# Optimization experiments

Hardware: AMD Instinct MI355X
Metric: run time of the kernel (lower is better)

The kernel has to match this reference:

```python
import jax, jax.numpy as jnp
import numpy as np

N = 500000
C_IN = 32
C_OUT = 64
K = 9  # neighbors per node


def setup_inputs() -> dict:
    key = jax.random.key(0)
    k1, k2, k3, k4 = jax.random.split(key, 4)
    features = jax.random.normal(k1, (N, C_IN), dtype=jnp.float32)
    # neighbor indices in [-1, N); -1 marks missing neighbor (zero-padded)
    neigh_idx = jax.random.randint(k2, (N, K), -1, N, dtype=jnp.int64)
    W = jax.random.normal(k3, (C_OUT, K * C_IN), dtype=jnp.float32) / np.sqrt(K * C_IN)
    b = jax.random.normal(k4, (C_OUT,), dtype=jnp.float32) * 0.01
    return {"features": features, "neigh_idx": neigh_idx, "W": W, "b": b}


def reference(features, neigh_idx, W, b):
    n = neigh_idx.shape[0]
    # append zero sentinel row at index n (matches torch cat with pad_vec)
    feat_padded = jnp.concatenate(
        [features, jnp.zeros((1, features.shape[1]), dtype=features.dtype)], axis=0
    )
    gather_idx = jnp.where(neigh_idx == -1, n, neigh_idx)
    gathered = feat_padded[gather_idx].reshape(n, -1)  # [N, 9*C]
    return gathered @ W.T + b
```

## Files before the change

### kernel.cpp

```cpp
#include <hip/hip_runtime.h>
#include <hip/hip_bf16.h>


typedef __bf16 bf16x8 __attribute__((ext_vector_type(8)));
typedef float  f32x16 __attribute__((ext_vector_type(16)));
typedef float  f32x4  __attribute__((ext_vector_type(4)));
typedef unsigned short ushort8 __attribute__((ext_vector_type(8)));

#define NPB 128

__global__ __launch_bounds__(256) void cvt_bf16_kernel(
    const float* __restrict__ src, __bf16* __restrict__ dst, long long total)
{
    long long stride = (long long)gridDim.x * 256 * 8;
    for (long long i = ((long long)blockIdx.x * 256 + threadIdx.x) * 8;
         i + 7 < total; i += stride) {
        f32x4 f0 = __builtin_nontemporal_load((const f32x4*)(src + i));
        f32x4 f1 = __builtin_nontemporal_load((const f32x4*)(src + i + 4));
        bf16x8 v;
        v[0] = (__bf16)f0[0]; v[1] = (__bf16)f0[1]; v[2] = (__bf16)f0[2]; v[3] = (__bf16)f0[3];
        v[4] = (__bf16)f1[0]; v[5] = (__bf16)f1[1]; v[6] = (__bf16)f1[2]; v[7] = (__bf16)f1[3];
        *(bf16x8*)(dst + i) = v;
    }
}

template<bool FAST>
__global__ __launch_bounds__(512, 8) void quadconv_kernel(
    const float*  __restrict__ feat,
    const __bf16* __restrict__ fb,
    const int*    __restrict__ nidx,
    const float*  __restrict__ Wm,
    const float*  __restrict__ bias,
    float*        __restrict__ out,
    int N)
{
    __shared__ __bf16 Wl[2304 * 8];

    const int tid  = threadIdx.x;
    const int lane = tid & 63;
    const int w    = tid >> 6;

    #pragma unroll
    for (int i = 0; i < 5; ++i) {
        int c = tid + i * 512;
        if (c < 2304) {
            int kk   = c >> 7;
            int r    = c & 127;
            int half = r >> 6;
            int l    = r & 63;
            int row  = half * 32 + (l & 31);
            int col0 = kk * 16 + (l >> 5) * 8;
            const float* wp = Wm + row * 288 + col0;
            f32x4 w0 = *(const f32x4*)(wp);
            f32x4 w1 = *(const f32x4*)(wp + 4);
            bf16x8 v;
            v[0] = (__bf16)w0[0]; v[1] = (__bf16)w0[1]; v[2] = (__bf16)w0[2]; v[3] = (__bf16)w0[3];
            v[4] = (__bf16)w1[0]; v[5] = (__bf16)w1[1]; v[6] = (__bf16)w1[2]; v[7] = (__bf16)w1[3];
            *(bf16x8*)&Wl[c * 8] = v;
        }
    }

    const int half    = w & 1;
    const int nodeOff = (w >> 1) * 32;
    const int klane   = (lane >> 5) * 8;
    const long long nbase = (long long)blockIdx.x * NPB + nodeOff;
    const long long row   = nbase + (lane & 31);
    const bool valid = row < (long long)N;

    const float bv = bias[half * 32 + (lane & 31)];

    int idxs[9];
    #pragma unroll
    for (int j = 0; j < 9; ++j)
        idxs[j] = valid ? nidx[row * 9 + j] : -1;

    __syncthreads();

    f32x16 acc;
    #pragma unroll
    for (int i = 0; i < 16; ++i) acc[i] = 0.0f;

    bf16x8 zvec;
    #pragma unroll
    for (int i = 0; i < 8; ++i) zvec[i] = (__bf16)0.0f;

    #pragma unroll 1
    for (int g = 0; g < 3; ++g) {
        bf16x8 a[6];
        #pragma unroll
        for (int jj = 0; jj < 3; ++jj) {
            int id = idxs[g * 3 + jj];
            #pragma unroll
            for (int h = 0; h < 2; ++h) {
                bf16x8 v = zvec;
                if (id >= 0) {
                    if (FAST) {
                        v = *(const bf16x8*)(fb + (long long)id * 32 + h * 16 + klane);
                    } else {
                        const float* sp = feat + (long long)id * 32 + h * 16 + klane;
                        f32x4 f0 = *(const f32x4*)(sp);
                        f32x4 f1 = *(const f32x4*)(sp + 4);
                        v[0] = (__bf16)f0[0]; v[1] = (__bf16)f0[1]; v[2] = (__bf16)f0[2]; v[3] = (__bf16)f0[3];
                        v[4] = (__bf16)f1[0]; v[5] = (__bf16)f1[1]; v[6] = (__bf16)f1[2]; v[7] = (__bf16)f1[3];
                    }
                }
                a[jj * 2 + h] = v;
            }
        }
        #pragma unroll
        for (int jj = 0; jj < 3; ++jj) {
            #pragma unroll
            for (int h = 0; h < 2; ++h) {
                int kk = g * 6 + jj * 2 + h;
                bf16x8 b = *(const bf16x8*)&Wl[((kk * 2 + half) * 64 + lane) * 8];
                acc = __builtin_amdgcn_mfma_f32_32x32x16_bf16(a[jj * 2 + h], b, acc, 0, 0, 0);
            }
        }
    }

    const int hi  = lane >> 5;
    const int col = half * 32 + (lane & 31);
    #pragma unroll
    for (int reg = 0; reg < 16; ++reg) {
        int m = (reg & 3) + 4 * hi + 8 * (reg >> 2);
        long long node = nbase + m;
        if (node < (long long)N) {
            out[node * 64 + col] = acc[reg] + bv;
        }
    }
}

extern "C" void kernel_launch(void* const* d_in, const int* in_sizes, int n_in,
                              void* d_out, int out_size, void* d_ws, size_t ws_size,
                              hipStream_t stream) {
    const float* feat = (const float*)d_in[0];
    const int*   nidx = (const int*)d_in[1];
    const float* Wm   = (const float*)d_in[2];
    const float* bias = (const float*)d_in[3];
    float*       out  = (float*)d_out;

    int N = in_sizes[0] / 32;
    long long total = (long long)N * 32;
    int grid = (N + NPB - 1) / NPB;

    if (ws_size >= (size_t)(total * sizeof(__bf16))) {
        __bf16* fb = (__bf16*)d_ws;
        cvt_bf16_kernel<<<2048, 256, 0, stream>>>(feat, fb, total);
        quadconv_kernel<true><<<grid, 512, 0, stream>>>(feat, fb, nidx, Wm, bias, out, N);
    } else {
        quadconv_kernel<false><<<grid, 512, 0, stream>>>(feat, nullptr, nidx, Wm, bias, out, N);
    }
}
```

Baseline: 309.5 us.

## Double-buffer neighbor gathers across MFMA groups and relax occupancy bound

Replaces the rolled three-iteration gather-then-MFMA loop with an explicit software pipeline: two groups of neighbor rows are loaded up front, and the third group's gather is issued while the first group's MFMAs run. The aim is to hide gather latency behind matrix math inside each wave. Because this holds more live vector registers, the launch bound drops from 8 to 6 waves per SIMD, which lowers occupancy. Neighbor index loads also become nontemporal loads so they do not pollute the cache.

```diff
diff --git a/kernel.cpp b/kernel.cpp
--- a/kernel.cpp
+++ b/kernel.cpp
@@ -5,7 +5,6 @@
 typedef __bf16 bf16x8 __attribute__((ext_vector_type(8)));
 typedef float  f32x16 __attribute__((ext_vector_type(16)));
 typedef float  f32x4  __attribute__((ext_vector_type(4)));
-typedef unsigned short ushort8 __attribute__((ext_vector_type(8)));
 
 #define NPB 128
 
@@ -25,7 +24,46 @@
 }
 
 template<bool FAST>
-__global__ __launch_bounds__(512, 8) void quadconv_kernel(
+__device__ __forceinline__ void load_group(
+    bf16x8 (&A)[6], const int (&idxs)[9], int g,
+    const __bf16* __restrict__ fb, const float* __restrict__ feat,
+    int klane, bf16x8 zvec)
+{
+    #pragma unroll
+    for (int jj = 0; jj < 3; ++jj) {
+        int id = idxs[g * 3 + jj];
+        #pragma unroll
+        for (int h = 0; h < 2; ++h) {
+            bf16x8 v = zvec;
+            if (id >= 0) {
+                if (FAST) {
+                    v = *(const bf16x8*)(fb + (long long)id * 32 + h * 16 + klane);
+                } else {
+                    const float* sp = feat + (long long)id * 32 + h * 16 + klane;
+                    f32x4 f0 = *(const f32x4*)(sp);
+                    f32x4 f1 = *(const f32x4*)(sp + 4);
+                    v[0] = (__bf16)f0[0]; v[1] = (__bf16)f0[1]; v[2] = (__bf16)f0[2]; v[3] = (__bf16)f0[3];
+                    v[4] = (__bf16)f1[0]; v[5] = (__bf16)f1[1]; v[6] = (__bf16)f1[2]; v[7] = (__bf16)f1[3];
+                }
+            }
+            A[jj * 2 + h] = v;
+        }
+    }
+}
+
+__device__ __forceinline__ void mfma_group(
+    f32x16& acc, const bf16x8 (&A)[6], const __bf16* Wl, int g, int half, int lane)
+{
+    #pragma unroll
+    for (int t = 0; t < 6; ++t) {
+        int kk = g * 6 + t;
+        bf16x8 b = *(const bf16x8*)&Wl[((kk * 2 + half) * 64 + lane) * 8];
+        acc = __builtin_amdgcn_mfma_f32_32x32x16_bf16(A[t], b, acc, 0, 0, 0);
+    }
+}
+
+template<bool FAST>
+__global__ __launch_bounds__(512, 6) void quadconv_kernel(
     const float*  __restrict__ feat,
     const __bf16* __restrict__ fb,
     const int*    __restrict__ nidx,
@@ -72,7 +110,7 @@
     int idxs[9];
     #pragma unroll
     for (int j = 0; j < 9; ++j)
-        idxs[j] = valid ? nidx[row * 9 + j] : -1;
+        idxs[j] = valid ? __builtin_nontemporal_load(nidx + row * 9 + j) : -1;
 
     __syncthreads();
 
@@ -84,39 +122,13 @@
     #pragma unroll
     for (int i = 0; i < 8; ++i) zvec[i] = (__bf16)0.0f;
 
-    #pragma unroll 1
-    for (int g = 0; g < 3; ++g) {
-        bf16x8 a[6];
-        #pragma unroll
-        for (int jj = 0; jj < 3; ++jj) {
-            int id = idxs[g * 3 + jj];
-            #pragma unroll
-            for (int h = 0; h < 2; ++h) {
-                bf16x8 v = zvec;
-                if (id >= 0) {
-                    if (FAST) {
-                        v = *(const bf16x8*)(fb + (long long)id * 32 + h * 16 + klane);
-                    } else {
-                        const float* sp = feat + (long long)id * 32 + h * 16 + klane;
-                        f32x4 f0 = *(const f32x4*)(sp);
-                        f32x4 f1 = *(const f32x4*)(sp + 4);
-                        v[0] = (__bf16)f0[0]; v[1] = (__bf16)f0[1]; v[2] = (__bf16)f0[2]; v[3] = (__bf16)f0[3];
-                        v[4] = (__bf16)f1[0]; v[5] = (__bf16)f1[1]; v[6] = (__bf16)f1[2]; v[7] = (__bf16)f1[3];
-                    }
-                }
-                a[jj * 2 + h] = v;
-            }
-        }
-        #pragma unroll
-        for (int jj = 0; jj < 3; ++jj) {
-            #pragma unroll
-            for (int h = 0; h < 2; ++h) {
-                int kk = g * 6 + jj * 2 + h;
-                bf16x8 b = *(const bf16x8*)&Wl[((kk * 2 + half) * 64 + lane) * 8];
-                acc = __builtin_amdgcn_mfma_f32_32x32x16_bf16(a[jj * 2 + h], b, acc, 0, 0, 0);
-            }
-        }
-    }
+    bf16x8 a0[6], a1[6];
+    load_group<FAST>(a0, idxs, 0, fb, feat, klane, zvec);
+    load_group<FAST>(a1, idxs, 1, fb, feat, klane, zvec);
+    mfma_group(acc, a0, Wl, 0, half, lane);
+    load_group<FAST>(a0, idxs, 2, fb, feat, klane, zvec);
+    mfma_group(acc, a1, Wl, 1, half, lane);
+    mfma_group(acc, a0, Wl, 2, half, lane);
 
     const int hi  = lane >> 5;
     const int col = half * 32 + (lane & 31);
```

Result: no change. 306.3 us (-1.0%).

## Permute bf16 feature layout for 32-byte gathers and software-pipeline neighbor loads

Applied to the files above, without the earlier changes.

The conversion kernel now writes each 32-channel bf16 row in a permuted chunk order, so each lane can fetch its two 8-element MFMA operands with a single 32-byte load instead of two 16-byte loads. The gather/MFMA loop is unrolled into a software pipeline that keeps two neighbor groups in flight before issuing MFMAs. Occupancy hint drops from 8 to 4 blocks to allow more registers for the prefetched operands, and neighbor-index loads become nontemporal. The trade is lower occupancy and a layout coupling between the two kernels.

```diff
diff --git a/kernel.cpp b/kernel.cpp
--- a/kernel.cpp
+++ b/kernel.cpp
@@ -2,10 +2,10 @@
 #include <hip/hip_bf16.h>
 
 
-typedef __bf16 bf16x8 __attribute__((ext_vector_type(8)));
-typedef float  f32x16 __attribute__((ext_vector_type(16)));
-typedef float  f32x4  __attribute__((ext_vector_type(4)));
-typedef unsigned short ushort8 __attribute__((ext_vector_type(8)));
+typedef __bf16 bf16x8  __attribute__((ext_vector_type(8)));
+typedef __bf16 bf16x16 __attribute__((ext_vector_type(16)));
+typedef float  f32x16  __attribute__((ext_vector_type(16)));
+typedef float  f32x4   __attribute__((ext_vector_type(4)));
 
 #define NPB 128
 
@@ -20,12 +20,59 @@
         bf16x8 v;
         v[0] = (__bf16)f0[0]; v[1] = (__bf16)f0[1]; v[2] = (__bf16)f0[2]; v[3] = (__bf16)f0[3];
         v[4] = (__bf16)f1[0]; v[5] = (__bf16)f1[1]; v[6] = (__bf16)f1[2]; v[7] = (__bf16)f1[3];
-        *(bf16x8*)(dst + i) = v;
+        long long row = i >> 5;
+        int q = (int)((i >> 3) & 3);
+        int p = ((q << 1) | (q >> 1)) & 3;
+        *(bf16x8*)(dst + row * 32 + p * 8) = v;
     }
 }
 
 template<bool FAST>
-__global__ __launch_bounds__(512, 8) void quadconv_kernel(
+__device__ __forceinline__ void load_rows(
+    bf16x16 (&A)[3], const int (&idxs)[9], int g,
+    const __bf16* __restrict__ fb, const float* __restrict__ feat,
+    int hi, bf16x16 zvec)
+{
+    #pragma unroll
+    for (int jj = 0; jj < 3; ++jj) {
+        int id = idxs[g * 3 + jj];
+        bf16x16 v = zvec;
+        if (id >= 0) {
+            if (FAST) {
+                v = *(const bf16x16*)(fb + (long long)id * 32 + hi * 16);
+            } else {
+                const float* sp = feat + (long long)id * 32;
+                f32x4 f0 = *(const f32x4*)(sp + hi * 8);
+                f32x4 f1 = *(const f32x4*)(sp + hi * 8 + 4);
+                f32x4 f2 = *(const f32x4*)(sp + 16 + hi * 8);
+                f32x4 f3 = *(const f32x4*)(sp + 16 + hi * 8 + 4);
+                v[0]  = (__bf16)f0[0]; v[1]  = (__bf16)f0[1]; v[2]  = (__bf16)f0[2]; v[3]  = (__bf16)f0[3];
+                v[4]  = (__bf16)f1[0]; v[5]  = (__bf16)f1[1]; v[6]  = (__bf16)f1[2]; v[7]  = (__bf16)f1[3];
+                v[8]  = (__bf16)f2[0]; v[9]  = (__bf16)f2[1]; v[10] = (__bf16)f2[2]; v[11] = (__bf16)f2[3];
+                v[12] = (__bf16)f3[0]; v[13] = (__bf16)f3[1]; v[14] = (__bf16)f3[2]; v[15] = (__bf16)f3[3];
+            }
+        }
+        A[jj] = v;
+    }
+}
+
+__device__ __forceinline__ void mfma_rows(
+    f32x16& acc, const bf16x16 (&A)[3], const __bf16* Wl, int g, int half, int lane)
+{
+    #pragma unroll
+    for (int jj = 0; jj < 3; ++jj) {
+        int kk = (g * 3 + jj) * 2;
+        bf16x8 lo = __builtin_shufflevector(A[jj], A[jj], 0, 1, 2, 3, 4, 5, 6, 7);
+        bf16x8 hi = __builtin_shufflevector(A[jj], A[jj], 8, 9, 10, 11, 12, 13, 14, 15);
+        bf16x8 b0 = *(const bf16x8*)&Wl[((kk * 2 + half) * 64 + lane) * 8];
+        acc = __builtin_amdgcn_mfma_f32_32x32x16_bf16(lo, b0, acc, 0, 0, 0);
+        bf16x8 b1 = *(const bf16x8*)&Wl[(((kk + 1) * 2 + half) * 64 + lane) * 8];
+        acc = __builtin_amdgcn_mfma_f32_32x32x16_bf16(hi, b1, acc, 0, 0, 0);
+    }
+}
+
+template<bool FAST>
+__global__ __launch_bounds__(512, 4) void quadconv_kernel(
     const float*  __restrict__ feat,
     const __bf16* __restrict__ fb,
     const int*    __restrict__ nidx,
@@ -62,7 +109,7 @@
 
     const int half    = w & 1;
     const int nodeOff = (w >> 1) * 32;
-    const int klane   = (lane >> 5) * 8;
+    const int hi      = lane >> 5;
     const long long nbase = (long long)blockIdx.x * NPB + nodeOff;
     const long long row   = nbase + (lane & 31);
     const bool valid = row < (long long)N;
@@ -72,7 +119,7 @@
     int idxs[9];
     #pragma unroll
     for (int j = 0; j < 9; ++j)
-        idxs[j] = valid ? nidx[row * 9 + j] : -1;
+        idxs[j] = valid ? __builtin_nontemporal_load(nidx + row * 9 + j) : -1;
 
     __syncthreads();
 
@@ -80,45 +127,18 @@
     #pragma unroll
     for (int i = 0; i < 16; ++i) acc[i] = 0.0f;
 
-    bf16x8 zvec;
+    bf16x16 zvec;
     #pragma unroll
-    for (int i = 0; i < 8; ++i) zvec[i] = (__bf16)0.0f;
+    for (int i = 0; i < 16; ++i) zvec[i] = (__bf16)0.0f;
 
-    #pragma unroll 1
-    for (int g = 0; g < 3; ++g) {
-        bf16x8 a[6];
-        #pragma unroll
-        for (int jj = 0; jj < 3; ++jj) {
-            int id = idxs[g * 3 + jj];
-            #pragma unroll
-            for (int h = 0; h < 2; ++h) {
-                bf16x8 v = zvec;
-                if (id >= 0) {
-                    if (FAST) {
-                        v = *(const bf16x8*)(fb + (long long)id * 32 + h * 16 + klane);
-                    } else {
-                        const float* sp = feat + (long long)id * 32 + h * 16 + klane;
-                        f32x4 f0 = *(const f32x4*)(sp);
-                        f32x4 f1 = *(const f32x4*)(sp + 4);
-                        v[0] = (__bf16)f0[0]; v[1] = (__bf16)f0[1]; v[2] = (__bf16)f0[2]; v[3] = (__bf16)f0[3];
-                        v[4] = (__bf16)f1[0]; v[5] = (__bf16)f1[1]; v[6] = (__bf16)f1[2]; v[7] = (__bf16)f1[3];
-                    }
-                }
-                a[jj * 2 + h] = v;
-            }
-        }
-        #pragma unroll
-        for (int jj = 0; jj < 3; ++jj) {
-            #pragma unroll
-            for (int h = 0; h < 2; ++h) {
-                int kk = g * 6 + jj * 2 + h;
-                bf16x8 b = *(const bf16x8*)&Wl[((kk * 2 + half) * 64 + lane) * 8];
-                acc = __builtin_amdgcn_mfma_f32_32x32x16_bf16(a[jj * 2 + h], b, acc, 0, 0, 0);
-            }
-        }
-    }
+    bf16x16 a0[3], a1[3];
+    load_rows<FAST>(a0, idxs, 0, fb, feat, hi, zvec);
+    load_rows<FAST>(a1, idxs, 1, fb, feat, hi, zvec);
+    mfma_rows(acc, a0, Wl, 0, half, lane);
+    load_rows<FAST>(a0, idxs, 2, fb, feat, hi, zvec);
+    mfma_rows(acc, a1, Wl, 1, half, lane);
+    mfma_rows(acc, a0, Wl, 2, half, lane);
 
-    const int hi  = lane >> 5;
     const int col = half * 32 + (lane & 31);
     #pragma unroll
     for (int reg = 0; reg < 16; ++reg) {
```

Measured after the change: 295.1 us. 4.6% less time.

## Switch to 16x16x32 MFMA tiles with per-wave full output columns

Applied to the files above, without the earlier changes.

Replaces the 32x32x16 MFMA layout, where pairs of waves split the output columns, with 16x16x32 MFMAs. Each wave now owns 16 nodes and all 64 output columns, so each neighbor feature row is gathered once per wave instead of twice. All nine gathers are issued up front, the weight LDS layout is rearranged to match, the index loads become nontemporal, and the occupancy hint drops from 8 to 4. The cost is more registers held live for the gathered rows and accumulators.

```diff
diff --git a/kernel.cpp b/kernel.cpp
--- a/kernel.cpp
+++ b/kernel.cpp
@@ -3,9 +3,7 @@
 
 
 typedef __bf16 bf16x8 __attribute__((ext_vector_type(8)));
-typedef float  f32x16 __attribute__((ext_vector_type(16)));
 typedef float  f32x4  __attribute__((ext_vector_type(4)));
-typedef unsigned short ushort8 __attribute__((ext_vector_type(8)));
 
 #define NPB 128
 
@@ -25,7 +23,7 @@
 }
 
 template<bool FAST>
-__global__ __launch_bounds__(512, 8) void quadconv_kernel(
+__global__ __launch_bounds__(512, 4) void quadconv_kernel(
     const float*  __restrict__ feat,
     const __bf16* __restrict__ fb,
     const int*    __restrict__ nidx,
@@ -39,18 +37,19 @@
     const int tid  = threadIdx.x;
     const int lane = tid & 63;
     const int w    = tid >> 6;
+    const int c4   = lane >> 4;
+    const int n16  = lane & 15;
 
     #pragma unroll
     for (int i = 0; i < 5; ++i) {
         int c = tid + i * 512;
         if (c < 2304) {
-            int kk   = c >> 7;
-            int r    = c & 127;
-            int half = r >> 6;
-            int l    = r & 63;
-            int row  = half * 32 + (l & 31);
-            int col0 = kk * 16 + (l >> 5) * 8;
-            const float* wp = Wm + row * 288 + col0;
+            int j = c >> 8;
+            int t = (c >> 6) & 3;
+            int l = c & 63;
+            int col = t * 16 + (l & 15);
+            int k0  = j * 32 + (l >> 4) * 8;
+            const float* wp = Wm + col * 288 + k0;
             f32x4 w0 = *(const f32x4*)(wp);
             f32x4 w1 = *(const f32x4*)(wp + 4);
             bf16x8 v;
@@ -60,72 +59,65 @@
         }
     }
 
-    const int half    = w & 1;
-    const int nodeOff = (w >> 1) * 32;
-    const int klane   = (lane >> 5) * 8;
-    const long long nbase = (long long)blockIdx.x * NPB + nodeOff;
-    const long long row   = nbase + (lane & 31);
-    const bool valid = row < (long long)N;
+    const long long nb   = (long long)blockIdx.x * NPB + w * 16;
+    const long long node = nb + n16;
+    const bool valid = node < (long long)N;
 
-    const float bv = bias[half * 32 + (lane & 31)];
+    float bv[4];
+    #pragma unroll
+    for (int t = 0; t < 4; ++t) bv[t] = bias[t * 16 + n16];
 
     int idxs[9];
     #pragma unroll
     for (int j = 0; j < 9; ++j)
-        idxs[j] = valid ? nidx[row * 9 + j] : -1;
+        idxs[j] = valid ? __builtin_nontemporal_load(nidx + node * 9 + j) : -1;
 
     __syncthreads();
-
-    f32x16 acc;
-    #pragma unroll
-    for (int i = 0; i < 16; ++i) acc[i] = 0.0f;
 
     bf16x8 zvec;
     #pragma unroll
     for (int i = 0; i < 8; ++i) zvec[i] = (__bf16)0.0f;
 
-    #pragma unroll 1
-    for (int g = 0; g < 3; ++g) {
-        bf16x8 a[6];
-        #pragma unroll
-        for (int jj = 0; jj < 3; ++jj) {
-            int id = idxs[g * 3 + jj];
-            #pragma unroll
-            for (int h = 0; h < 2; ++h) {
-                bf16x8 v = zvec;
-                if (id >= 0) {
-                    if (FAST) {
-                        v = *(const bf16x8*)(fb + (long long)id * 32 + h * 16 + klane);
-                    } else {
-                        const float* sp = feat + (long long)id * 32 + h * 16 + klane;
-                        f32x4 f0 = *(const f32x4*)(sp);
-                        f32x4 f1 = *(const f32x4*)(sp + 4);
-                        v[0] = (__bf16)f0[0]; v[1] = (__bf16)f0[1]; v[2] = (__bf16)f0[2]; v[3] = (__bf16)f0[3];
-                        v[4] = (__bf16)f1[0]; v[5] = (__bf16)f1[1]; v[6] = (__bf16)f1[2]; v[7] = (__bf16)f1[3];
-                    }
-                }
-                a[jj * 2 + h] = v;
+    bf16x8 a[9];
+    #pragma unroll
+    for (int j = 0; j < 9; ++j) {
+        bf16x8 v = zvec;
+        int id = idxs[j];
+        if (id >= 0) {
+            if (FAST) {
+                v = *(const bf16x8*)(fb + (long long)id * 32 + c4 * 8);
+            } else {
+                const float* sp = feat + (long long)id * 32 + c4 * 8;
+                f32x4 f0 = *(const f32x4*)(sp);
+                f32x4 f1 = *(const f32x4*)(sp + 4);
+                v[0] = (__bf16)f0[0]; v[1] = (__bf16)f0[1]; v[2] = (__bf16)f0[2]; v[3] = (__bf16)f0[3];
+                v[4] = (__bf16)f1[0]; v[5] = (__bf16)f1[1]; v[6] = (__bf16)f1[2]; v[7] = (__bf16)f1[3];
             }
         }
+        a[j] = v;
+    }
+
+    f32x4 acc[4];
+    #pragma unroll
+    for (int t = 0; t < 4; ++t) { acc[t][0] = 0.f; acc[t][1] = 0.f; acc[t][2] = 0.f; acc[t][3] = 0.f; }
+
+    #pragma unroll
+    for (int j = 0; j < 9; ++j) {
         #pragma unroll
-        for (int jj = 0; jj < 3; ++jj) {
-            #pragma unroll
-            for (int h = 0; h < 2; ++h) {
-                int kk = g * 6 + jj * 2 + h;
-                bf16x8 b = *(const bf16x8*)&Wl[((kk * 2 + half) * 64 + lane) * 8];
-                acc = __builtin_amdgcn_mfma_f32_32x32x16_bf16(a[jj * 2 + h], b, acc, 0, 0, 0);
-            }
+        for (int t = 0; t < 4; ++t) {
+            bf16x8 b = *(const bf16x8*)&Wl[((j * 4 + t) * 64 + lane) * 8];
+            acc[t] = __builtin_amdgcn_mfma_f32_16x16x32_bf16(a[j], b, acc[t], 0, 0, 0);
         }
     }
 
-    const int hi  = lane >> 5;
-    const int col = half * 32 + (lane & 31);
     #pragma unroll
-    for (int reg = 0; reg < 16; ++reg) {
-        int m = (reg & 3) + 4 * hi + 8 * (reg >> 2);
-        long long node = nbase + m;
-        if (node < (long long)N) {
-            out[node * 64 + col] = acc[reg] + bv;
+    for (int reg = 0; reg < 4; ++reg) {
+        long long nd = nb + c4 * 4 + reg;
+        if (nd < (long long)N) {
+            #pragma unroll
+            for (int t = 0; t < 4; ++t) {
+                out[nd * 64 + t * 16 + n16] = acc[t][reg] + bv[t];
+            }
         }
     }
 }
```

Result: faster. 286.4 us (-7.5%).
